# Performance work log

Measured on AMD Instinct MI355X. Metric: run time of the kernel, lower is better.

The kernel has to match this reference:

```python
import jax, jax.numpy as jnp
import numpy as np

B, H, W, S, C = 16, 128, 128, 4, 64
SC = S * C
SK_ITERS, SK_EPS = 20, 1e-6


def setup_inputs() -> dict:
    key = jax.random.key(0)
    ks = jax.random.split(key, 12)
    x = jax.random.normal(ks[0], (B, H, W, S, C), dtype=jnp.float32)
    # torch Linear weights are [out, in], kaiming-uniform-ish scale ~ 1/sqrt(in)
    w_pre = jax.random.normal(ks[1], (S, SC), dtype=jnp.float32) / np.sqrt(SC)
    w_post = jax.random.normal(ks[2], (S, SC), dtype=jnp.float32) / np.sqrt(SC)
    w_res = jax.random.normal(ks[3], (S * S, SC), dtype=jnp.float32) / np.sqrt(SC)
    b_pre = jax.random.normal(ks[4], (1, S), dtype=jnp.float32) * 0.01
    b_res = jax.random.normal(ks[5], (S * S,), dtype=jnp.float32) * 0.01
    b_post = jax.random.normal(ks[6], (1, S), dtype=jnp.float32) * 0.01
    alpha_pre = jax.random.normal(ks[7], (1,), dtype=jnp.float32) * 0.01
    alpha_res = jax.random.normal(ks[8], (1,), dtype=jnp.float32) * 0.01
    alpha_post = jax.random.normal(ks[9], (1,), dtype=jnp.float32) * 0.01
    rms_w = jnp.ones((SC,), dtype=jnp.float32)
    # conv kernel HWIO for 3x3 same-padded Conv2d(C, C, bias=False)
    conv_w = jax.random.normal(ks[10], (3, 3, C, C), dtype=jnp.float32) / np.sqrt(9 * C)
    return {"x": x, "w_pre": w_pre, "w_post": w_post, "w_res": w_res,
            "b_pre": b_pre, "b_res": b_res, "b_post": b_post,
            "alpha_pre": alpha_pre, "alpha_res": alpha_res, "alpha_post": alpha_post,
            "rms_w": rms_w, "conv_w": conv_w}


def _sinkhorn(h_tilde):
    # h_tilde: [B,H,W,S,S]; stable softmax-style shift then 20 row/col rescales
    h = h_tilde - h_tilde.max(axis=(-2, -1), keepdims=True)
    h = jnp.exp(h)
    def body(_, h):
        h = h / (h.sum(axis=-2, keepdims=True) + SK_EPS)
        h = h / (h.sum(axis=-1, keepdims=True) + SK_EPS)
        return h
    return jax.lax.fori_loop(0, SK_ITERS, body, h)


def reference(x, w_pre, w_post, w_res, b_pre, b_res, b_post,
              alpha_pre, alpha_res, alpha_post, rms_w, conv_w):
    s = b_pre.shape[-1]
    x_arrow = x.reshape(*x.shape[:-2], -1)           # [B,H,W,S*C]
    eps = jnp.finfo(x.dtype).eps                     # torch RMSNorm default eps
    x_norm = x_arrow * jax.lax.rsqrt(jnp.mean(x_arrow * x_arrow, axis=-1, keepdims=True) + eps)
    x_norm = x_norm * rms_w

    h_tilde_pre = alpha_pre * (x_norm @ w_pre.T) + b_pre          # [B,H,W,S]
    h_tilde_post = alpha_post * (x_norm @ w_post.T) + b_post       # [B,H,W,S]
    h_tilde_res = alpha_res * (x_norm @ w_res.T).reshape(*x.shape[:-2], s, s) \
                  + b_res.reshape(s, s)                            # [B,H,W,S,S]

    h_pre = jax.nn.sigmoid(h_tilde_pre)                            # [B,H,W,S]
    h_res = _sinkhorn(h_tilde_res)                                 # [B,H,W,S,S]
    h_post = 2.0 * jax.nn.sigmoid(h_tilde_post)                    # [B,H,W,S]

    # x_pre = h_pre @ x (pre-mix across streams) -> [B,H,W,C]
    x_pre = jnp.einsum('bhws,bhwsc->bhwc', h_pre, x)
    # layer: Conv2d(C,C,3,padding=1,bias=False), applied in NHWC directly
    layer_out = jax.lax.conv_general_dilated(
        x_pre, conv_w, window_strides=(1, 1), padding='SAME',
        dimension_numbers=('NHWC', 'HWIO', 'NHWC'))                # [B,H,W,C]

    out = jnp.einsum('bhwst,bhwtc->bhwsc', h_res, x) \
          + h_post[..., :, None] * layer_out[..., None, :]         # [B,H,W,S,C]
    return out
```

## Files before the change

### kernel.cpp

```cpp
#include <hip/hip_runtime.h>
#include <cstdint>
#include <cstring>

typedef unsigned int u32;
typedef unsigned short u16;
typedef __attribute__((ext_vector_type(8))) __bf16 bf16x8;
typedef __attribute__((ext_vector_type(4))) float f32x4;

#define DEV static __device__ __forceinline__

DEV float bf2f(u16 v){ u32 u = ((u32)v)<<16; float f; __builtin_memcpy(&f,&u,4); return f; }
DEV u16 f2bf(float f){ u32 u; __builtin_memcpy(&u,&f,4); u32 r = u + 0x7fffu + ((u>>16)&1u); return (u16)(r>>16); }
DEV void unpk(u32 v, float& lo, float& hi){
  u32 a = v<<16; u32 b = v & 0xffff0000u;
  __builtin_memcpy(&lo,&a,4); __builtin_memcpy(&hi,&b,4);
}
DEV u32 pk2(float lo, float hi){ return (u32)f2bf(lo) | (((u32)f2bf(hi))<<16); }
DEV float fsigm(float x){ return __builtin_amdgcn_rcpf(1.f + __expf(-x)); }
DEV f32x4 MFMA16(uint4 a, uint4 b, f32x4 c){
  return __builtin_amdgcn_mfma_f32_16x16x32_bf16(
      __builtin_bit_cast(bf16x8, a), __builtin_bit_cast(bf16x8, b), c, 0, 0, 0);
}

DEV bool detect_bf16(const void* rmsw){ return ((const u16*)rmsw)[0] == 0x3F80u; }

DEV u32 rnd1(u32 f){ return (f + 0x7fffu + ((f>>16)&1u)) >> 16; }
DEV u32 rnd2(u32 lo, u32 hi){ return rnd1(lo) | (rnd1(hi)<<16); }

DEV uint4 load8(const void* p, size_t idx8, bool bf){
  if (bf) return ((const uint4*)p)[idx8];
  const uint4* q = (const uint4*)p;
  uint4 a = q[2*idx8], b = q[2*idx8+1];
  return make_uint4(rnd2(a.x,a.y), rnd2(a.z,a.w), rnd2(b.x,b.y), rnd2(b.z,b.w));
}
DEV void store8(void* p, size_t idx8, bool bf, const float* v){
  if (bf){
    ((uint4*)p)[idx8] = make_uint4(pk2(v[0],v[1]),pk2(v[2],v[3]),pk2(v[4],v[5]),pk2(v[6],v[7]));
  } else {
    float4* q = (float4*)p;
    q[2*idx8]   = make_float4(v[0],v[1],v[2],v[3]);
    q[2*idx8+1] = make_float4(v[4],v[5],v[6],v[7]);
  }
}
DEV float ldsc(const void* p, int i, bool bf){
  return bf ? bf2f(((const u16*)p)[i]) : ((const float*)p)[i];
}

__global__ __launch_bounds__(256) void prepack_kernel(
    const void* __restrict__ wpre, const void* __restrict__ wpost,
    const void* __restrict__ wres, const void* __restrict__ rmsw,
    const void* __restrict__ convw, u16* __restrict__ wsW, u16* __restrict__ wsC)
{
  const bool bf = detect_bf16(rmsw);
  int tid = blockIdx.x*256 + threadIdx.x;
  if (tid < 8192){
    int i = tid & 7, lane = (tid>>3)&63, nt = (tid>>9)&1, kk = tid>>10;
    int j = nt*16 + (lane&15);
    int k = kk*32 + ((lane>>4)<<3) + i;
    float v = 0.f;
    if (j < 4)       v = ldsc(wpre, j*256+k, bf);
    else if (j < 8)  v = ldsc(wpost, (j-4)*256+k, bf);
    else if (j < 24) v = ldsc(wres, (j-8)*256+k, bf);
    v *= ldsc(rmsw, k, bf);
    wsW[tid] = f2bf(v);
  }
  if (tid < 36864){
    int i = tid & 7, lane = (tid>>3)&63, nt = (tid>>9)&3, kk = tid>>11;
    int co = nt*16 + (lane&15);
    int k = kk*32 + ((lane>>4)<<3) + i;
    wsC[tid] = f2bf(ldsc(convw, k*64+co, bf));
  }
}

__global__ __launch_bounds__(256,2) void mHC_fused_kernel(
    const void* __restrict__ x,
    const void* __restrict__ bpre, const void* __restrict__ bres, const void* __restrict__ bpost,
    const void* __restrict__ apre, const void* __restrict__ ares, const void* __restrict__ apost,
    const void* __restrict__ rmsw,
    const u16* __restrict__ wsW, const u16* __restrict__ wsC,
    void* __restrict__ out)
{
  __shared__ __align__(16) u16 s_xpre[18*18*68];
  __shared__ __align__(16) u16 s_h[256*20];
  __shared__ __align__(16) u16 s_hpre[4][64];
  __shared__ __align__(16) u16 s_L[4][16*68];

  const bool bf = detect_bf16(rmsw);
  const int tid = threadIdx.x;
  const int wave = tid>>6, lane = tid&63;
  const int mm = lane&15, q = lane>>4;
  const int blk = blockIdx.x;
  const int bimg = blk>>6, ty = (blk>>3)&7, tx = blk&7;
  const size_t xb8 = (size_t)bimg*16384*32;
  const int gy0 = ty*16-1, gx0 = tx*16-1;

  const float a_pre = ldsc(apre,0,bf), a_res = ldsc(ares,0,bf), a_post = ldsc(apost,0,bf);
  const float al0 = (mm<4)? a_pre : (mm<8)? a_post : a_res;
  const float bi0 = (mm<4)? ldsc(bpre,mm,bf) : (mm<8)? ldsc(bpost,mm-4,bf) : ldsc(bres,mm-8,bf);
  const float al1 = a_res;
  const float bi1 = (mm<8)? ldsc(bres,mm+8,bf) : 0.f;

  const uint4* wWv = reinterpret_cast<const uint4*>(wsW);
  const uint4* wCv = reinterpret_cast<const uint4*>(wsC);

  uint4 Ax[4][8];
  {
    const int gx = tx*16 + mm;
    #pragma unroll
    for (int i=0;i<4;i++){
      const int gy = ty*16 + wave*4 + i;
      const size_t p8 = xb8 + (size_t)(gy*128 + gx)*32;
      #pragma unroll
      for (int kk=0;kk<8;kk++) Ax[i][kk] = load8(x, p8 + kk*4+q, bf);
    }
  }

  #pragma unroll
  for (int i=0;i<4;i++){
    float ssq = 0.f;
    #pragma unroll
    for (int kk=0;kk<8;kk++){
      const u32 vv[4] = {Ax[i][kk].x,Ax[i][kk].y,Ax[i][kk].z,Ax[i][kk].w};
      #pragma unroll
      for (int w2=0;w2<4;w2++){ float lo,hi; unpk(vv[w2],lo,hi);
        ssq = __builtin_fmaf(lo,lo,ssq); ssq = __builtin_fmaf(hi,hi,ssq); }
    }
    ssq += __shfl_xor(ssq,16);
    ssq += __shfl_xor(ssq,32);
    const float scale = __builtin_amdgcn_rsqf(ssq*(1.f/256.f) + 1.1920928955078125e-07f);
    float rs[4];
    #pragma unroll
    for (int r=0;r<4;r++) rs[r] = __shfl(scale, q*4+r);

    f32x4 D0 = {0.f,0.f,0.f,0.f}, D1 = {0.f,0.f,0.f,0.f};
    #pragma unroll
    for (int kk=0;kk<8;kk++){
      D0 = MFMA16(Ax[i][kk], wWv[(kk*2+0)*64+lane], D0);
      D1 = MFMA16(Ax[i][kk], wWv[(kk*2+1)*64+lane], D1);
    }
    #pragma unroll
    for (int r=0;r<4;r++){
      const float ht0 = __builtin_fmaf(al0*rs[r], D0[r], bi0);
      const float ht1 = __builtin_fmaf(al1*rs[r], D1[r], bi1);
      if (mm < 4) s_hpre[wave][(q*4+r)*4+mm] = f2bf(fsigm(ht0));
      const int pid = (wave*4+i)*16 + (q*4+r);
      if (mm < 8) s_h[pid*20 + mm+8] = f2bf(ht1);
      else        s_h[pid*20 + mm-8] = f2bf(ht0);
      if (mm>=4 && mm<8) s_h[pid*20 + 12 + mm] = f2bf(2.f*fsigm(ht0));
    }
    __builtin_amdgcn_wave_barrier();
    {
      float hp[4];
      { const uint2 hv = *reinterpret_cast<const uint2*>(&s_hpre[wave][mm*4]);
        unpk(hv.x, hp[0], hp[1]); unpk(hv.y, hp[2], hp[3]); }
      float xa[8] = {0,0,0,0,0,0,0,0}, xb[8] = {0,0,0,0,0,0,0,0};
      #pragma unroll
      for (int kk=0;kk<8;kk++){
        const float h = hp[kk>>1];
        const u32 vv[4] = {Ax[i][kk].x,Ax[i][kk].y,Ax[i][kk].z,Ax[i][kk].w};
        #pragma unroll
        for (int w2=0;w2<4;w2++){
          float lo,hi; unpk(vv[w2],lo,hi);
          if (kk&1){ xb[2*w2]  =__builtin_fmaf(h,lo,xb[2*w2]);  xb[2*w2+1]=__builtin_fmaf(h,hi,xb[2*w2+1]); }
          else     { xa[2*w2]  =__builtin_fmaf(h,lo,xa[2*w2]);  xa[2*w2+1]=__builtin_fmaf(h,hi,xa[2*w2+1]); }
        }
      }
      const int pix = (wave*4+i+1)*18 + (mm+1);
      uint2* dA = reinterpret_cast<uint2*>(&s_xpre[pix*68 + 8*q]);
      dA[0] = make_uint2(pk2(xa[0],xa[1]), pk2(xa[2],xa[3]));
      dA[1] = make_uint2(pk2(xa[4],xa[5]), pk2(xa[6],xa[7]));
      uint2* dB = reinterpret_cast<uint2*>(&s_xpre[pix*68 + 32 + 8*q]);
      dB[0] = make_uint2(pk2(xb[0],xb[1]), pk2(xb[2],xb[3]));
      dB[1] = make_uint2(pk2(xb[4],xb[5]), pk2(xb[6],xb[7]));
    }
    __builtin_amdgcn_wave_barrier();
  }

  #pragma unroll
  for (int hp_=0; hp_<2; ++hp_){
    const bool pv = hp_ ? (mm==0) : true;
    const int hx = hp_ ? (64+wave) : (wave*16+mm);
    int ey, ex;
    if (hx < 18)      { ey = 0;       ex = hx;      }
    else if (hx < 36) { ey = 17;      ex = hx-18;   }
    else if (hx < 52) { ey = hx-35;   ex = 0;       }
    else              { ey = hx-51;   ex = 17;      }
    const int gy = gy0+ey, gx = gx0+ex;
    const bool inimg = pv && ((u32)gy < 128u) && ((u32)gx < 128u);
    const size_t p8 = xb8 + (size_t)(u32)(gy*128 + gx)*32;

    uint4 A[8];
    #pragma unroll
    for (int kk=0;kk<8;kk++){
      uint4 v = make_uint4(0u,0u,0u,0u);
      if (inimg) v = load8(x, p8 + kk*4+q, bf);
      A[kk] = v;
    }
    float ssq = 0.f;
    #pragma unroll
    for (int kk=0;kk<8;kk++){
      const u32 vv[4] = {A[kk].x,A[kk].y,A[kk].z,A[kk].w};
      #pragma unroll
      for (int w2=0;w2<4;w2++){ float lo,hi; unpk(vv[w2],lo,hi);
        ssq = __builtin_fmaf(lo,lo,ssq); ssq = __builtin_fmaf(hi,hi,ssq); }
    }
    ssq += __shfl_xor(ssq,16);
    ssq += __shfl_xor(ssq,32);
    const float scale = __builtin_amdgcn_rsqf(ssq*(1.f/256.f) + 1.1920928955078125e-07f);
    float rs[4];
    #pragma unroll
    for (int r=0;r<4;r++) rs[r] = __shfl(scale, q*4+r);

    f32x4 D0 = {0.f,0.f,0.f,0.f};
    #pragma unroll
    for (int kk=0;kk<8;kk++) D0 = MFMA16(A[kk], wWv[(kk*2+0)*64+lane], D0);

    #pragma unroll
    for (int r=0;r<4;r++){
      if (mm < 4){
        const float ht0 = __builtin_fmaf(al0*rs[r], D0[r], bi0);
        s_hpre[wave][(q*4+r)*4+mm] = f2bf(fsigm(ht0));
      }
    }
    __builtin_amdgcn_wave_barrier();
    if (pv){
      float hp[4];
      { const uint2 hv = *reinterpret_cast<const uint2*>(&s_hpre[wave][mm*4]);
        unpk(hv.x, hp[0], hp[1]); unpk(hv.y, hp[2], hp[3]); }
      float xa[8] = {0,0,0,0,0,0,0,0}, xb[8] = {0,0,0,0,0,0,0,0};
      #pragma unroll
      for (int kk=0;kk<8;kk++){
        const float h = hp[kk>>1];
        const u32 vv[4] = {A[kk].x,A[kk].y,A[kk].z,A[kk].w};
        #pragma unroll
        for (int w2=0;w2<4;w2++){
          float lo,hi; unpk(vv[w2],lo,hi);
          if (kk&1){ xb[2*w2]  =__builtin_fmaf(h,lo,xb[2*w2]);  xb[2*w2+1]=__builtin_fmaf(h,hi,xb[2*w2+1]); }
          else     { xa[2*w2]  =__builtin_fmaf(h,lo,xa[2*w2]);  xa[2*w2+1]=__builtin_fmaf(h,hi,xa[2*w2+1]); }
        }
      }
      const int pix = ey*18 + ex;
      uint2* dA = reinterpret_cast<uint2*>(&s_xpre[pix*68 + 8*q]);
      dA[0] = make_uint2(pk2(xa[0],xa[1]), pk2(xa[2],xa[3]));
      dA[1] = make_uint2(pk2(xa[4],xa[5]), pk2(xa[6],xa[7]));
      uint2* dB = reinterpret_cast<uint2*>(&s_xpre[pix*68 + 32 + 8*q]);
      dB[0] = make_uint2(pk2(xb[0],xb[1]), pk2(xb[2],xb[3]));
      dB[1] = make_uint2(pk2(xb[4],xb[5]), pk2(xb[6],xb[7]));
    }
    __builtin_amdgcn_wave_barrier();
  }
  __syncthreads();

  {
    const int p = tid;
    float h[16];
    const uint2* h2 = reinterpret_cast<const uint2*>(&s_h[p*20]);
    #pragma unroll
    for (int e=0;e<4;e++){ const uint2 v = h2[e];
      unpk(v.x,h[4*e],h[4*e+1]); unpk(v.y,h[4*e+2],h[4*e+3]); }
    float mx = h[0];
    #pragma unroll
    for (int e=1;e<16;e++) mx = fmaxf(mx,h[e]);
    #pragma unroll
    for (int e=0;e<16;e++) h[e] = __expf(h[e]-mx);
    for (int it=0; it<20; ++it){
      #pragma unroll
      for (int t=0;t<4;t++){
        const float rc = __builtin_amdgcn_rcpf((h[t]+h[4+t])+(h[8+t]+h[12+t]) + 1e-6f);
        h[t]*=rc; h[4+t]*=rc; h[8+t]*=rc; h[12+t]*=rc;
      }
      #pragma unroll
      for (int s=0;s<4;s++){
        const float rc = __builtin_amdgcn_rcpf((h[4*s]+h[4*s+1])+(h[4*s+2]+h[4*s+3]) + 1e-6f);
        h[4*s]*=rc; h[4*s+1]*=rc; h[4*s+2]*=rc; h[4*s+3]*=rc;
      }
    }
    uint2* hw = reinterpret_cast<uint2*>(&s_h[p*20]);
    #pragma unroll
    for (int e=0;e<4;e++) hw[e] = make_uint2(pk2(h[4*e],h[4*e+1]), pk2(h[4*e+2],h[4*e+3]));
  }
  __syncthreads();

  #pragma unroll
  for (int i=0;i<4;i++){
    const int py = wave*4+i;
    f32x4 D[4];
    #pragma unroll
    for (int nt=0;nt<4;nt++) D[nt] = (f32x4){0.f,0.f,0.f,0.f};
    #pragma unroll
    for (int kk=0;kk<18;kk++){
      const int tq  = 4*kk+q;
      const int tap = tq>>3;
      const int ci0 = (tq&7)*8;
      const int dy = tap/3, dx = tap-3*dy;
      const int pix = (py+dy)*18 + (mm+dx);
      const uint2* a2 = reinterpret_cast<const uint2*>(&s_xpre[pix*68 + ci0]);
      const uint2 alo = a2[0], ahi = a2[1];
      const uint4 av = make_uint4(alo.x, alo.y, ahi.x, ahi.y);
      #pragma unroll
      for (int nt=0;nt<4;nt++)
        D[nt] = MFMA16(av, wCv[(kk*4+nt)*64+lane], D[nt]);
    }
    __builtin_amdgcn_wave_barrier();
    #pragma unroll
    for (int nt=0;nt<4;nt++)
      #pragma unroll
      for (int r=0;r<4;r++)
        s_L[wave][(q*4+r)*68 + nt*16 + mm] = f2bf(D[nt][r]);
    __builtin_amdgcn_wave_barrier();

    const int gy = ty*16+py, gx = tx*16+mm;
    float xa[4][8], xb[4][8];
    #pragma unroll
    for (int t=0;t<4;t++){
      const u32 va[4] = {Ax[i][2*t].x,Ax[i][2*t].y,Ax[i][2*t].z,Ax[i][2*t].w};
      const u32 vb[4] = {Ax[i][2*t+1].x,Ax[i][2*t+1].y,Ax[i][2*t+1].z,Ax[i][2*t+1].w};
      #pragma unroll
      for (int w2=0;w2<4;w2++){
        unpk(va[w2], xa[t][2*w2], xa[t][2*w2+1]);
        unpk(vb[w2], xb[t][2*w2], xb[t][2*w2+1]);
      }
    }
    const int pid = py*16+mm;
    float hr[16], hpo[4];
    {
      const uint2* h2 = reinterpret_cast<const uint2*>(&s_h[pid*20]);
      #pragma unroll
      for (int e=0;e<4;e++){ const uint2 v = h2[e];
        unpk(v.x,hr[4*e],hr[4*e+1]); unpk(v.y,hr[4*e+2],hr[4*e+3]); }
      const uint2 v4 = h2[4];
      unpk(v4.x,hpo[0],hpo[1]); unpk(v4.y,hpo[2],hpo[3]);
    }
    float LA[8], LB[8];
    {
      const uint2* lA = reinterpret_cast<const uint2*>(&s_L[wave][mm*68 + 8*q]);
      const uint2* lB = reinterpret_cast<const uint2*>(&s_L[wave][mm*68 + 32 + 8*q]);
      const uint2 a0v=lA[0], a1v=lA[1], b0v=lB[0], b1v=lB[1];
      unpk(a0v.x,LA[0],LA[1]); unpk(a0v.y,LA[2],LA[3]);
      unpk(a1v.x,LA[4],LA[5]); unpk(a1v.y,LA[6],LA[7]);
      unpk(b0v.x,LB[0],LB[1]); unpk(b0v.y,LB[2],LB[3]);
      unpk(b1v.x,LB[4],LB[5]); unpk(b1v.y,LB[6],LB[7]);
    }
    const size_t ob8 = ((size_t)bimg*16384 + (size_t)(gy*128+gx))*32;
    #pragma unroll
    for (int s=0;s<4;s++){
      float oA[8], oB[8];
      #pragma unroll
      for (int j2=0;j2<8;j2++){ oA[j2]=hpo[s]*LA[j2]; oB[j2]=hpo[s]*LB[j2]; }
      #pragma unroll
      for (int t=0;t<4;t++){
        const float w0 = hr[4*s+t];
        #pragma unroll
        for (int j2=0;j2<8;j2++){
          oA[j2]=__builtin_fmaf(w0,xa[t][j2],oA[j2]);
          oB[j2]=__builtin_fmaf(w0,xb[t][j2],oB[j2]);
        }
      }
      store8(out, ob8 + s*8 + q,     bf, oA);
      store8(out, ob8 + s*8 + 4 + q, bf, oB);
    }
  }
}

extern "C" void kernel_launch(void* const* d_in, const int* in_sizes, int n_in,
                              void* d_out, int out_size, void* d_ws, size_t ws_size,
                              hipStream_t stream)
{
  const void* x     = d_in[0];
  const void* wpre  = d_in[1];
  const void* wpost = d_in[2];
  const void* wres  = d_in[3];
  const void* bpre  = d_in[4];
  const void* bres  = d_in[5];
  const void* bpost = d_in[6];
  const void* apre  = d_in[7];
  const void* ares  = d_in[8];
  const void* apost = d_in[9];
  const void* rmsw  = d_in[10];
  const void* convw = d_in[11];
  u16* wsW = (u16*)d_ws;
  u16* wsC = wsW + 8192;

  hipLaunchKernelGGL(prepack_kernel, dim3(144), dim3(256), 0, stream,
                     wpre, wpost, wres, rmsw, convw, wsW, wsC);
  hipLaunchKernelGGL(mHC_fused_kernel, dim3(1024), dim3(256), 0, stream,
                     x, bpre, bres, bpost, apre, ares, apost, rmsw, wsW, wsC, d_out);
}
```

Baseline: 698.0 us.

## Halve spatial tile to 8x16 and reload x in epilogue to raise occupancy

The fused kernel now handles an 8x16 pixel tile per block instead of 16x16, doubling the grid and shrinking the LDS buffers. It no longer keeps the block's x rows in registers between the pre-mix phase and the output phase; it reloads them from global memory after the conv MFMAs. Launch bounds go from 2 to 4 blocks per SIMD to raise occupancy. In exchange, the halo overhead per tile grows, from 324 to 180 staged pixels for half as many interior pixels. x is also read twice per interior pixel, and only half the threads run Sinkhorn.

```diff
diff --git a/kernel.cpp b/kernel.cpp
--- a/kernel.cpp
+++ b/kernel.cpp
@@ -72,7 +72,7 @@
   }
 }
 
-__global__ __launch_bounds__(256,2) void mHC_fused_kernel(
+__global__ __launch_bounds__(256,4) void mHC_fused_kernel(
     const void* __restrict__ x,
     const void* __restrict__ bpre, const void* __restrict__ bres, const void* __restrict__ bpost,
     const void* __restrict__ apre, const void* __restrict__ ares, const void* __restrict__ apost,
@@ -80,8 +80,8 @@
     const u16* __restrict__ wsW, const u16* __restrict__ wsC,
     void* __restrict__ out)
 {
-  __shared__ __align__(16) u16 s_xpre[18*18*68];
-  __shared__ __align__(16) u16 s_h[256*20];
+  __shared__ __align__(16) u16 s_xpre[10*18*68];
+  __shared__ __align__(16) u16 s_h[128*20];
   __shared__ __align__(16) u16 s_hpre[4][64];
   __shared__ __align__(16) u16 s_L[4][16*68];
 
@@ -90,9 +90,9 @@
   const int wave = tid>>6, lane = tid&63;
   const int mm = lane&15, q = lane>>4;
   const int blk = blockIdx.x;
-  const int bimg = blk>>6, ty = (blk>>3)&7, tx = blk&7;
+  const int bimg = blk>>7, ty = (blk>>3)&15, tx = blk&7;
   const size_t xb8 = (size_t)bimg*16384*32;
-  const int gy0 = ty*16-1, gx0 = tx*16-1;
+  const int gy0 = ty*8-1, gx0 = tx*16-1;
 
   const float a_pre = ldsc(apre,0,bf), a_res = ldsc(ares,0,bf), a_post = ldsc(apost,0,bf);
   const float al0 = (mm<4)? a_pre : (mm<8)? a_post : a_res;
@@ -103,24 +103,19 @@
   const uint4* wWv = reinterpret_cast<const uint4*>(wsW);
   const uint4* wCv = reinterpret_cast<const uint4*>(wsC);
 
-  uint4 Ax[4][8];
-  {
-    const int gx = tx*16 + mm;
-    #pragma unroll
-    for (int i=0;i<4;i++){
-      const int gy = ty*16 + wave*4 + i;
-      const size_t p8 = xb8 + (size_t)(gy*128 + gx)*32;
-      #pragma unroll
-      for (int kk=0;kk<8;kk++) Ax[i][kk] = load8(x, p8 + kk*4+q, bf);
-    }
-  }
-
   #pragma unroll
-  for (int i=0;i<4;i++){
+  for (int i=0;i<2;i++){
+    const int iy = wave*2 + i;
+    const int gy = ty*8 + iy, gx = tx*16 + mm;
+    const size_t p8 = xb8 + (size_t)(gy*128 + gx)*32;
+    uint4 A[8];
+    #pragma unroll
+    for (int kk=0;kk<8;kk++) A[kk] = load8(x, p8 + kk*4+q, bf);
+
     float ssq = 0.f;
     #pragma unroll
     for (int kk=0;kk<8;kk++){
-      const u32 vv[4] = {Ax[i][kk].x,Ax[i][kk].y,Ax[i][kk].z,Ax[i][kk].w};
+      const u32 vv[4] = {A[kk].x,A[kk].y,A[kk].z,A[kk].w};
       #pragma unroll
       for (int w2=0;w2<4;w2++){ float lo,hi; unpk(vv[w2],lo,hi);
         ssq = __builtin_fmaf(lo,lo,ssq); ssq = __builtin_fmaf(hi,hi,ssq); }
@@ -135,95 +130,21 @@
     f32x4 D0 = {0.f,0.f,0.f,0.f}, D1 = {0.f,0.f,0.f,0.f};
     #pragma unroll
     for (int kk=0;kk<8;kk++){
-      D0 = MFMA16(Ax[i][kk], wWv[(kk*2+0)*64+lane], D0);
-      D1 = MFMA16(Ax[i][kk], wWv[(kk*2+1)*64+lane], D1);
+      D0 = MFMA16(A[kk], wWv[(kk*2+0)*64+lane], D0);
+      D1 = MFMA16(A[kk], wWv[(kk*2+1)*64+lane], D1);
     }
     #pragma unroll
     for (int r=0;r<4;r++){
       const float ht0 = __builtin_fmaf(al0*rs[r], D0[r], bi0);
       const float ht1 = __builtin_fmaf(al1*rs[r], D1[r], bi1);
       if (mm < 4) s_hpre[wave][(q*4+r)*4+mm] = f2bf(fsigm(ht0));
-      const int pid = (wave*4+i)*16 + (q*4+r);
+      const int pid = iy*16 + (q*4+r);
       if (mm < 8) s_h[pid*20 + mm+8] = f2bf(ht1);
       else        s_h[pid*20 + mm-8] = f2bf(ht0);
       if (mm>=4 && mm<8) s_h[pid*20 + 12 + mm] = f2bf(2.f*fsigm(ht0));
     }
     __builtin_amdgcn_wave_barrier();
     {
-      float hp[4];
-      { const uint2 hv = *reinterpret_cast<const uint2*>(&s_hpre[wave][mm*4]);
-        unpk(hv.x, hp[0], hp[1]); unpk(hv.y, hp[2], hp[3]); }
-      float xa[8] = {0,0,0,0,0,0,0,0}, xb[8] = {0,0,0,0,0,0,0,0};
-      #pragma unroll
-      for (int kk=0;kk<8;kk++){
-        const float h = hp[kk>>1];
-        const u32 vv[4] = {Ax[i][kk].x,Ax[i][kk].y,Ax[i][kk].z,Ax[i][kk].w};
-        #pragma unroll
-        for (int w2=0;w2<4;w2++){
-          float lo,hi; unpk(vv[w2],lo,hi);
-          if (kk&1){ xb[2*w2]  =__builtin_fmaf(h,lo,xb[2*w2]);  xb[2*w2+1]=__builtin_fmaf(h,hi,xb[2*w2+1]); }
-          else     { xa[2*w2]  =__builtin_fmaf(h,lo,xa[2*w2]);  xa[2*w2+1]=__builtin_fmaf(h,hi,xa[2*w2+1]); }
-        }
-      }
-      const int pix = (wave*4+i+1)*18 + (mm+1);
-      uint2* dA = reinterpret_cast<uint2*>(&s_xpre[pix*68 + 8*q]);
-      dA[0] = make_uint2(pk2(xa[0],xa[1]), pk2(xa[2],xa[3]));
-      dA[1] = make_uint2(pk2(xa[4],xa[5]), pk2(xa[6],xa[7]));
-      uint2* dB = reinterpret_cast<uint2*>(&s_xpre[pix*68 + 32 + 8*q]);
-      dB[0] = make_uint2(pk2(xb[0],xb[1]), pk2(xb[2],xb[3]));
-      dB[1] = make_uint2(pk2(xb[4],xb[5]), pk2(xb[6],xb[7]));
-    }
-    __builtin_amdgcn_wave_barrier();
-  }
-
-  #pragma unroll
-  for (int hp_=0; hp_<2; ++hp_){
-    const bool pv = hp_ ? (mm==0) : true;
-    const int hx = hp_ ? (64+wave) : (wave*16+mm);
-    int ey, ex;
-    if (hx < 18)      { ey = 0;       ex = hx;      }
-    else if (hx < 36) { ey = 17;      ex = hx-18;   }
-    else if (hx < 52) { ey = hx-35;   ex = 0;       }
-    else              { ey = hx-51;   ex = 17;      }
-    const int gy = gy0+ey, gx = gx0+ex;
-    const bool inimg = pv && ((u32)gy < 128u) && ((u32)gx < 128u);
-    const size_t p8 = xb8 + (size_t)(u32)(gy*128 + gx)*32;
-
-    uint4 A[8];
-    #pragma unroll
-    for (int kk=0;kk<8;kk++){
-      uint4 v = make_uint4(0u,0u,0u,0u);
-      if (inimg) v = load8(x, p8 + kk*4+q, bf);
-      A[kk] = v;
-    }
-    float ssq = 0.f;
-    #pragma unroll
-    for (int kk=0;kk<8;kk++){
-      const u32 vv[4] = {A[kk].x,A[kk].y,A[kk].z,A[kk].w};
-      #pragma unroll
-      for (int w2=0;w2<4;w2++){ float lo,hi; unpk(vv[w2],lo,hi);
-        ssq = __builtin_fmaf(lo,lo,ssq); ssq = __builtin_fmaf(hi,hi,ssq); }
-    }
-    ssq += __shfl_xor(ssq,16);
-    ssq += __shfl_xor(ssq,32);
-    const float scale = __builtin_amdgcn_rsqf(ssq*(1.f/256.f) + 1.1920928955078125e-07f);
-    float rs[4];
-    #pragma unroll
-    for (int r=0;r<4;r++) rs[r] = __shfl(scale, q*4+r);
-
-    f32x4 D0 = {0.f,0.f,0.f,0.f};
-    #pragma unroll
-    for (int kk=0;kk<8;kk++) D0 = MFMA16(A[kk], wWv[(kk*2+0)*64+lane], D0);
-
-    #pragma unroll
-    for (int r=0;r<4;r++){
-      if (mm < 4){
-        const float ht0 = __builtin_fmaf(al0*rs[r], D0[r], bi0);
-        s_hpre[wave][(q*4+r)*4+mm] = f2bf(fsigm(ht0));
-      }
-    }
-    __builtin_amdgcn_wave_barrier();
-    if (pv){
       float hp[4];
       { const uint2 hv = *reinterpret_cast<const uint2*>(&s_hpre[wave][mm*4]);
         unpk(hv.x, hp[0], hp[1]); unpk(hv.y, hp[2], hp[3]); }
@@ -239,6 +160,79 @@
           else     { xa[2*w2]  =__builtin_fmaf(h,lo,xa[2*w2]);  xa[2*w2+1]=__builtin_fmaf(h,hi,xa[2*w2+1]); }
         }
       }
+      const int pix = (iy+1)*18 + (mm+1);
+      uint2* dA = reinterpret_cast<uint2*>(&s_xpre[pix*68 + 8*q]);
+      dA[0] = make_uint2(pk2(xa[0],xa[1]), pk2(xa[2],xa[3]));
+      dA[1] = make_uint2(pk2(xa[4],xa[5]), pk2(xa[6],xa[7]));
+      uint2* dB = reinterpret_cast<uint2*>(&s_xpre[pix*68 + 32 + 8*q]);
+      dB[0] = make_uint2(pk2(xb[0],xb[1]), pk2(xb[2],xb[3]));
+      dB[1] = make_uint2(pk2(xb[4],xb[5]), pk2(xb[6],xb[7]));
+    }
+    __builtin_amdgcn_wave_barrier();
+  }
+
+  {
+    const int hx = wave*16 + mm;
+    const bool pv = hx < 52;
+    int ey, ex;
+    if (hx < 18)      { ey = 0;       ex = hx;      }
+    else if (hx < 36) { ey = 9;       ex = hx-18;   }
+    else if (hx < 44) { ey = hx-35;   ex = 0;       }
+    else              { ey = hx-43;   ex = 17;      }
+    const int gy = gy0+ey, gx = gx0+ex;
+    const bool inimg = pv && ((u32)gy < 128u) && ((u32)gx < 128u);
+    const size_t p8 = xb8 + (size_t)(u32)(gy*128 + gx)*32;
+
+    uint4 A[8];
+    #pragma unroll
+    for (int kk=0;kk<8;kk++){
+      uint4 v = make_uint4(0u,0u,0u,0u);
+      if (inimg) v = load8(x, p8 + kk*4+q, bf);
+      A[kk] = v;
+    }
+    float ssq = 0.f;
+    #pragma unroll
+    for (int kk=0;kk<8;kk++){
+      const u32 vv[4] = {A[kk].x,A[kk].y,A[kk].z,A[kk].w};
+      #pragma unroll
+      for (int w2=0;w2<4;w2++){ float lo,hi; unpk(vv[w2],lo,hi);
+        ssq = __builtin_fmaf(lo,lo,ssq); ssq = __builtin_fmaf(hi,hi,ssq); }
+    }
+    ssq += __shfl_xor(ssq,16);
+    ssq += __shfl_xor(ssq,32);
+    const float scale = __builtin_amdgcn_rsqf(ssq*(1.f/256.f) + 1.1920928955078125e-07f);
+    float rs[4];
+    #pragma unroll
+    for (int r=0;r<4;r++) rs[r] = __shfl(scale, q*4+r);
+
+    f32x4 D0 = {0.f,0.f,0.f,0.f};
+    #pragma unroll
+    for (int kk=0;kk<8;kk++) D0 = MFMA16(A[kk], wWv[(kk*2+0)*64+lane], D0);
+
+    #pragma unroll
+    for (int r=0;r<4;r++){
+      if (mm < 4){
+        const float ht0 = __builtin_fmaf(al0*rs[r], D0[r], bi0);
+        s_hpre[wave][(q*4+r)*4+mm] = f2bf(fsigm(ht0));
+      }
+    }
+    __builtin_amdgcn_wave_barrier();
+    if (pv){
+      float hp[4];
+      { const uint2 hv = *reinterpret_cast<const uint2*>(&s_hpre[wave][mm*4]);
+        unpk(hv.x, hp[0], hp[1]); unpk(hv.y, hp[2], hp[3]); }
+      float xa[8] = {0,0,0,0,0,0,0,0}, xb[8] = {0,0,0,0,0,0,0,0};
+      #pragma unroll
+      for (int kk=0;kk<8;kk++){
+        const float h = hp[kk>>1];
+        const u32 vv[4] = {A[kk].x,A[kk].y,A[kk].z,A[kk].w};
+        #pragma unroll
+        for (int w2=0;w2<4;w2++){
+          float lo,hi; unpk(vv[w2],lo,hi);
+          if (kk&1){ xb[2*w2]  =__builtin_fmaf(h,lo,xb[2*w2]);  xb[2*w2+1]=__builtin_fmaf(h,hi,xb[2*w2+1]); }
+          else     { xa[2*w2]  =__builtin_fmaf(h,lo,xa[2*w2]);  xa[2*w2+1]=__builtin_fmaf(h,hi,xa[2*w2+1]); }
+        }
+      }
       const int pix = ey*18 + ex;
       uint2* dA = reinterpret_cast<uint2*>(&s_xpre[pix*68 + 8*q]);
       dA[0] = make_uint2(pk2(xa[0],xa[1]), pk2(xa[2],xa[3]));
@@ -251,7 +245,7 @@
   }
   __syncthreads();
 
-  {
+  if (tid < 128){
     const int p = tid;
     float h[16];
     const uint2* h2 = reinterpret_cast<const uint2*>(&s_h[p*20]);
@@ -282,8 +276,8 @@
   __syncthreads();
 
   #pragma unroll
-  for (int i=0;i<4;i++){
-    const int py = wave*4+i;
+  for (int i=0;i<2;i++){
+    const int py = wave*2+i;
     f32x4 D[4];
     #pragma unroll
     for (int nt=0;nt<4;nt++) D[nt] = (f32x4){0.f,0.f,0.f,0.f};
@@ -301,6 +295,12 @@
       for (int nt=0;nt<4;nt++)
         D[nt] = MFMA16(av, wCv[(kk*4+nt)*64+lane], D[nt]);
     }
+    const int gy = ty*8+py, gx = tx*16+mm;
+    const size_t p8 = xb8 + (size_t)(gy*128+gx)*32;
+    uint4 A[8];
+    #pragma unroll
+    for (int kk=0;kk<8;kk++) A[kk] = load8(x, p8 + kk*4+q, bf);
+
     __builtin_amdgcn_wave_barrier();
     #pragma unroll
     for (int nt=0;nt<4;nt++)
@@ -309,12 +309,11 @@
         s_L[wave][(q*4+r)*68 + nt*16 + mm] = f2bf(D[nt][r]);
     __builtin_amdgcn_wave_barrier();
 
-    const int gy = ty*16+py, gx = tx*16+mm;
     float xa[4][8], xb[4][8];
     #pragma unroll
     for (int t=0;t<4;t++){
-      const u32 va[4] = {Ax[i][2*t].x,Ax[i][2*t].y,Ax[i][2*t].z,Ax[i][2*t].w};
-      const u32 vb[4] = {Ax[i][2*t+1].x,Ax[i][2*t+1].y,Ax[i][2*t+1].z,Ax[i][2*t+1].w};
+      const u32 va[4] = {A[2*t].x,A[2*t].y,A[2*t].z,A[2*t].w};
+      const u32 vb[4] = {A[2*t+1].x,A[2*t+1].y,A[2*t+1].z,A[2*t+1].w};
       #pragma unroll
       for (int w2=0;w2<4;w2++){
         unpk(va[w2], xa[t][2*w2], xa[t][2*w2+1]);
@@ -383,6 +382,6 @@
 
   hipLaunchKernelGGL(prepack_kernel, dim3(144), dim3(256), 0, stream,
                      wpre, wpost, wres, rmsw, convw, wsW, wsC);
-  hipLaunchKernelGGL(mHC_fused_kernel, dim3(1024), dim3(256), 0, stream,
+  hipLaunchKernelGGL(mHC_fused_kernel, dim3(2048), dim3(256), 0, stream,
                      x, bpre, bres, bpost, apre, ares, apost, rmsw, wsW, wsC, d_out);
 }
```

Measured after the change: 662.9 us. 5.0% less time.
